# Kernel tuning notes

Measured on AMD Instinct MI355X. Metric: run time of the kernel, lower is better.

Reference implementation:

```python
import jax, jax.numpy as jnp
import numpy as np

IN_DIM, OUT_DIM = 96, 32
D = IN_DIM + OUT_DIM  # 128, feature dim of x
H, KQ = 8, 64         # head_num, KQ_dim
GAMMA = 1e-4


def setup_inputs() -> dict:
    key = jax.random.key(0)
    kx, kk, kq, kv = jax.random.split(key, 4)
    B, N = 32, 2048
    std_kq = (GAMMA / D) ** 0.5
    return {
        "x": jax.random.normal(kx, (B, N, D), dtype=jnp.float32),
        # nn.Linear weight shape [out_features, in_features]; stacked per head
        "Wk": jax.random.normal(kk, (H, KQ, D), dtype=jnp.float32) * std_kq,
        "Wq": jax.random.normal(kq, (H, KQ, D), dtype=jnp.float32) * std_kq,
        "Wv": jax.random.normal(kv, (H, D, D), dtype=jnp.float32) * GAMMA,
    }


def reference(x, Wk, Wq, Wv):
    # Per-head projections (nn.Linear: y = x @ W^T), stacked over heads h
    K = jnp.einsum("bnd,hkd->bhnk", x, Wk)  # [B,H,N,KQ]
    Q = jnp.einsum("bnd,hkd->bhnk", x, Wq)  # [B,H,N,KQ]
    V = jnp.einsum("bnd,hed->bhne", x, Wv)  # [B,H,N,D]
    # No softmax -> (Q K^T) V == Q (K^T V); use the O(n d^2) associative form
    KtV = jnp.einsum("bhnk,bhne->bhke", K, V)  # [B,H,KQ,D]
    # sum over heads folded into the contraction
    out = jnp.einsum("bhnk,bhke->bne", Q, KtV)  # [B,N,D]
    return out
```

## Files before the change

### kernel.cpp

```cpp
#include <hip/hip_runtime.h>

#define BB 32
#define NN 2048
#define DD 128
#define HH 8
#define KK 64

typedef __attribute__((ext_vector_type(8))) short bf16x8;
typedef __attribute__((ext_vector_type(4))) float f32x4;
#define MFMA_BF16 __builtin_amdgcn_mfma_f32_16x16x32_bf16


__device__ __forceinline__ float bf2f(unsigned short h){ return __uint_as_float(((unsigned)h) << 16); }
__device__ __forceinline__ unsigned short f2bf(float f){
  unsigned u = __float_as_uint(f);
  u += 0x7fffu + ((u >> 16) & 1u);
  return (unsigned short)(u >> 16);
}

__device__ __forceinline__ bf16x8 ldfrag_sw(const unsigned short* base, int row16, int kc, int lane){
  int d = row16 + (lane & 15);
  int q = lane >> 4;
  int ch = ((kc << 2) + q) ^ (d & 7);
  return *(const bf16x8*)(base + d*128 + ch*8);
}
__device__ __forceinline__ bf16x8 ldfrag_pad(const unsigned short* base, int row16, int kc, int lane){
  int r = row16 + (lane & 15);
  int q = lane >> 4;
  return *(const bf16x8*)(base + r*136 + kc*32 + q*8);
}

__global__ __launch_bounds__(256) void kgkp(const float* __restrict__ x,
                                            const float* __restrict__ Wq,
                                            const float* __restrict__ Wk,
                                            float* __restrict__ Gp,
                                            unsigned short* __restrict__ Pbf){
  __shared__ __align__(16) unsigned short sm[32768];
  const int t = threadIdx.x;
  const int bid = blockIdx.x;
  if (bid < 512){
    unsigned short* xh = sm;
    unsigned short* xl = sm + 16384;
    const int b = bid & 31, chunk = bid >> 5;
    const float* xb = x + ((size_t)b*NN + (size_t)chunk*128)*DD;
    for (int it = 0; it < 4; ++it){
      int gidx = it*256 + t;
      int n4g = (gidx & 7) | (((gidx >> 6) & 3) << 3);
      int dcq = ((gidx >> 3) & 7) | (((gidx >> 8) & 3) << 3);
      float4 v[4];
      #pragma unroll
      for (int j = 0; j < 4; ++j)
        v[j] = *(const float4*)(xb + (size_t)(n4g*4 + j)*DD + dcq*4);
      #pragma unroll
      for (int i = 0; i < 4; ++i){
        int d = dcq*4 + i;
        float f0 = (&v[0].x)[i], f1 = (&v[1].x)[i], f2 = (&v[2].x)[i], f3 = (&v[3].x)[i];
        unsigned short h0 = f2bf(f0), h1 = f2bf(f1), h2 = f2bf(f2), h3 = f2bf(f3);
        unsigned short l0 = f2bf(f0 - bf2f(h0)), l1 = f2bf(f1 - bf2f(h1));
        unsigned short l2 = f2bf(f2 - bf2f(h2)), l3 = f2bf(f3 - bf2f(h3));
        int off = d*128 + ((((n4g >> 1) ^ (d & 7)) << 3) + (n4g & 1)*4);
        *(ushort4*)(xh + off) = make_ushort4(h0, h1, h2, h3);
        *(ushort4*)(xl + off) = make_ushort4(l0, l1, l2, l3);
      }
    }
    __syncthreads();
    const int w = t >> 6, lane = t & 63, quad = lane >> 4;
    const int wr = (w >> 1)*64, wc = (w & 1)*64;
    f32x4 acc[4][4] = {};
    for (int kc = 0; kc < 4; ++kc){
      bf16x8 ah[4], al[4], bh[4], bl[4];
      #pragma unroll
      for (int r = 0; r < 4; ++r){
        ah[r] = ldfrag_sw(xh, wr + r*16, kc, lane);
        al[r] = ldfrag_sw(xl, wr + r*16, kc, lane);
      }
      #pragma unroll
      for (int c = 0; c < 4; ++c){
        bh[c] = ldfrag_sw(xh, wc + c*16, kc, lane);
        bl[c] = ldfrag_sw(xl, wc + c*16, kc, lane);
      }
      #pragma unroll
      for (int r = 0; r < 4; ++r)
        #pragma unroll
        for (int c = 0; c < 4; ++c){
          acc[r][c] = MFMA_BF16(ah[r], bh[c], acc[r][c], 0, 0, 0);
          acc[r][c] = MFMA_BF16(ah[r], bl[c], acc[r][c], 0, 0, 0);
          acc[r][c] = MFMA_BF16(al[r], bh[c], acc[r][c], 0, 0, 0);
        }
    }
    float* gp = Gp + ((size_t)(chunk*32 + b) << 14);
    #pragma unroll
    for (int r = 0; r < 4; ++r)
      #pragma unroll
      for (int c = 0; c < 4; ++c)
        #pragma unroll
        for (int reg = 0; reg < 4; ++reg)
          gp[(size_t)(wr + r*16 + quad*4 + reg)*DD + wc + c*16 + (lane & 15)] = acc[r][c][reg];
  } else {
    float* Aq = (float*)sm;
    float* Bk = Aq + 64*36;
    const int kpid = bid - 512;
    const int h = kpid >> 2, rt = kpid & 3;
    const int i0 = rt * 32;
    const int tr = t >> 5, tc = t & 31;
    const float* wq = Wq + h*KK*DD;
    const float* wk = Wk + h*KK*DD;
    for (int i = t; i < 512; i += 256){
      int k = i >> 3, c4 = (i & 7) << 2;
      *(float4*)(&Aq[k*36 + c4]) = *(const float4*)(wq + k*DD + i0 + c4);
    }
    for (int i = t; i < 2048; i += 256){
      int k = i >> 5, c4 = (i & 31) << 2;
      *(float4*)(&Bk[k*132 + c4]) = *(const float4*)(wk + k*DD + c4);
    }
    __syncthreads();
    float acc[4][4] = {};
    for (int k = 0; k < 64; k += 2){
      float a0[4], b0[4], a1[4], b1[4];
      *(float4*)a0 = *(float4*)(&Aq[k*36 + tr*4]);
      *(float4*)b0 = *(float4*)(&Bk[k*132 + tc*4]);
      *(float4*)a1 = *(float4*)(&Aq[(k+1)*36 + tr*4]);
      *(float4*)b1 = *(float4*)(&Bk[(k+1)*132 + tc*4]);
      #pragma unroll
      for (int i = 0; i < 4; ++i)
        #pragma unroll
        for (int j = 0; j < 4; ++j){
          acc[i][j] += a0[i]*b0[j];
          acc[i][j] += a1[i]*b1[j];
        }
    }
    unsigned short* Ph = Pbf + h*DD*DD;
    #pragma unroll
    for (int i = 0; i < 4; ++i)
      *(ushort4*)(&Ph[(i0 + tr*4 + i)*DD + tc*4]) =
          make_ushort4(f2bf(acc[i][0]), f2bf(acc[i][1]), f2bf(acc[i][2]), f2bf(acc[i][3]));
  }
}

__global__ __launch_bounds__(256) void kgr(const float* __restrict__ Gp,
                                           unsigned short* __restrict__ Gbf){
  size_t idx = (size_t)blockIdx.x*1024 + threadIdx.x*4;
  int b = (int)(idx >> 14); int i = (int)(idx & 16383);
  float4 s = make_float4(0.f, 0.f, 0.f, 0.f);
  #pragma unroll
  for (int p = 0; p < 16; ++p){
    float4 v = *(const float4*)(Gp + ((size_t)(p*32 + b) << 14) + i);
    s.x += v.x; s.y += v.y; s.z += v.z; s.w += v.w;
  }
  *(ushort4*)(Gbf + idx) = make_ushort4(f2bf(s.x), f2bf(s.y), f2bf(s.z), f2bf(s.w));
}

__global__ __launch_bounds__(256) void km(const unsigned short* __restrict__ Gbf,
                                          const float* __restrict__ Wv,
                                          const unsigned short* __restrict__ Pbf,
                                          float* __restrict__ Mpt){
  __shared__ __align__(16) unsigned short As[128*136];
  __shared__ __align__(16) unsigned short Bs[64*136];
  const int bid = blockIdx.x;
  const int b = bid & 31, h = (bid >> 5) & 7, eh = bid >> 8;
  const int e0 = eh * 64;
  const int t = threadIdx.x;
  const int w = t >> 6, lane = t & 63, quad = lane >> 4;
  const unsigned short* Gb = Gbf + ((size_t)b << 14);
  const float* Wvh = Wv + ((size_t)h*DD + e0)*DD;
  for (int i = t; i < 2048; i += 256){
    int r = i >> 4, ch = (i & 15) * 8;
    *(uint4*)(As + r*136 + ch) = *(const uint4*)(Gb + r*128 + ch);
  }
  for (int i = t; i < 2048; i += 256){
    int e = i >> 5, dc = (i & 31) * 4;
    float4 v = *(const float4*)(Wvh + (size_t)e*DD + dc);
    *(ushort4*)(Bs + e*136 + dc) = make_ushort4(f2bf(v.x), f2bf(v.y), f2bf(v.z), f2bf(v.w));
  }
  __syncthreads();
  const int wr = (w >> 1)*64, wc = (w & 1)*32;
  f32x4 acc1[4][2] = {};
  for (int kc = 0; kc < 4; ++kc){
    bf16x8 a[4], bb[2];
    #pragma unroll
    for (int r = 0; r < 4; ++r) a[r] = ldfrag_pad(As, wr + r*16, kc, lane);
    #pragma unroll
    for (int c = 0; c < 2; ++c) bb[c] = ldfrag_pad(Bs, wc + c*16, kc, lane);
    #pragma unroll
    for (int r = 0; r < 4; ++r)
      #pragma unroll
      for (int c = 0; c < 2; ++c)
        acc1[r][c] = MFMA_BF16(a[r], bb[c], acc1[r][c], 0, 0, 0);
  }
  __syncthreads();
  #pragma unroll
  for (int r = 0; r < 4; ++r)
    #pragma unroll
    for (int c = 0; c < 2; ++c){
      int e = wc + c*16 + (lane & 15);
      int c0 = wr + r*16 + quad*4;
      *(ushort4*)(Bs + e*136 + c0) = make_ushort4(f2bf(acc1[r][c][0]), f2bf(acc1[r][c][1]),
                                                  f2bf(acc1[r][c][2]), f2bf(acc1[r][c][3]));
    }
  const unsigned short* Ph = Pbf + h*DD*DD;
  for (int i = t; i < 2048; i += 256){
    int r = i >> 4, ch = (i & 15) * 8;
    *(uint4*)(As + r*136 + ch) = *(const uint4*)(Ph + r*128 + ch);
  }
  __syncthreads();
  f32x4 acc2[4][2] = {};
  for (int kc = 0; kc < 4; ++kc){
    bf16x8 a[4], bb[2];
    #pragma unroll
    for (int r = 0; r < 4; ++r) a[r] = ldfrag_pad(As, wr + r*16, kc, lane);
    #pragma unroll
    for (int c = 0; c < 2; ++c) bb[c] = ldfrag_pad(Bs, wc + c*16, kc, lane);
    #pragma unroll
    for (int r = 0; r < 4; ++r)
      #pragma unroll
      for (int c = 0; c < 2; ++c)
        acc2[r][c] = MFMA_BF16(a[r], bb[c], acc2[r][c], 0, 0, 0);
  }
  __syncthreads();
  float* Af = (float*)As;
  #pragma unroll
  for (int r = 0; r < 4; ++r)
    #pragma unroll
    for (int c = 0; c < 2; ++c){
      int e = wc + c*16 + (lane & 15);
      int d0 = wr + r*16 + quad*4;
      *(float4*)(Af + e*132 + d0) = make_float4(acc2[r][c][0], acc2[r][c][1], acc2[r][c][2], acc2[r][c][3]);
    }
  __syncthreads();
  float* Mb = Mpt + ((size_t)(b*8 + h) << 14);
  for (int i = t; i < 2048; i += 256){
    int e = i >> 5, dc = (i & 31) * 4;
    *(float4*)(Mb + (size_t)(e0 + e)*DD + dc) = *(const float4*)(Af + e*132 + dc);
  }
}

__global__ __launch_bounds__(256) void kmr(const float* __restrict__ Mpt,
                                           unsigned short* __restrict__ Mtbf){
  size_t idx = (size_t)blockIdx.x*1024 + threadIdx.x*4;
  int b = (int)(idx >> 14); int i = (int)(idx & 16383);
  float4 s = make_float4(0.f, 0.f, 0.f, 0.f);
  #pragma unroll
  for (int h = 0; h < 8; ++h){
    float4 v = *(const float4*)(Mpt + ((size_t)(b*8 + h) << 14) + i);
    s.x += v.x; s.y += v.y; s.z += v.z; s.w += v.w;
  }
  *(ushort4*)(Mtbf + idx) = make_ushort4(f2bf(s.x), f2bf(s.y), f2bf(s.z), f2bf(s.w));
}

__global__ __launch_bounds__(256) void ko(const float* __restrict__ x,
                                          const unsigned short* __restrict__ Mtbf,
                                          float* __restrict__ out){
  __shared__ __align__(16) unsigned short xs[16384];
  __shared__ __align__(16) unsigned short Ms[16384];
  const int bid = blockIdx.x;
  const int b = bid & 31, nt = bid >> 5;
  const int t = threadIdx.x;
  const int w = t >> 6, lane = t & 63, quad = lane >> 4;
  const float* xb = x + ((size_t)b*NN + (size_t)nt*128)*DD;
  const unsigned short* Mtb = Mtbf + ((size_t)b << 14);
  for (int i = t; i < 4096; i += 256){
    int n = i >> 5, dcq = i & 31;
    float4 v = *(const float4*)(xb + (size_t)n*DD + dcq*4);
    int off = n*128 + ((((dcq >> 1) ^ (n & 7)) << 3) + (dcq & 1)*4);
    *(ushort4*)(xs + off) = make_ushort4(f2bf(v.x), f2bf(v.y), f2bf(v.z), f2bf(v.w));
  }
  for (int i = t; i < 2048; i += 256){
    int e = i >> 4, ng = i & 15;
    *(uint4*)(Ms + e*128 + ((ng ^ (e & 7)) << 3)) = *(const uint4*)(Mtb + e*128 + ng*8);
  }
  __syncthreads();
  const int wr = (w >> 1)*64, wc = (w & 1)*64;
  f32x4 acc[4][4] = {};
  for (int kc = 0; kc < 4; ++kc){
    bf16x8 a[4], bb[4];
    #pragma unroll
    for (int r = 0; r < 4; ++r) a[r] = ldfrag_sw(xs, wr + r*16, kc, lane);
    #pragma unroll
    for (int c = 0; c < 4; ++c) bb[c] = ldfrag_sw(Ms, wc + c*16, kc, lane);
    #pragma unroll
    for (int r = 0; r < 4; ++r)
      #pragma unroll
      for (int c = 0; c < 4; ++c)
        acc[r][c] = MFMA_BF16(a[r], bb[c], acc[r][c], 0, 0, 0);
  }
  float* ob = out + ((size_t)b*NN + (size_t)nt*128)*DD;
  #pragma unroll
  for (int r = 0; r < 4; ++r)
    #pragma unroll
    for (int c = 0; c < 4; ++c)
      #pragma unroll
      for (int reg = 0; reg < 4; ++reg)
        ob[(size_t)(wr + r*16 + quad*4 + reg)*DD + wc + c*16 + (lane & 15)] = acc[r][c][reg];
}

extern "C" void kernel_launch(void* const* d_in, const int* in_sizes, int n_in,
                              void* d_out, int out_size, void* d_ws, size_t ws_size,
                              hipStream_t stream){
  const float* x  = (const float*)d_in[0];
  const float* Wk = (const float*)d_in[1];
  const float* Wq = (const float*)d_in[2];
  const float* Wv = (const float*)d_in[3];
  float* out = (float*)d_out;
  float* ws = (float*)d_ws;
  float* Gp  = ws;
  float* Mpt = ws + 8388608;
  unsigned short* Gbf  = (unsigned short*)(ws + 12582912);
  unsigned short* Pbf  = Gbf + 524288;
  unsigned short* Mtbf = Pbf + 131072;

  kgkp<<<544, 256, 0, stream>>>(x, Wq, Wk, Gp, Pbf);
  kgr <<<512, 256, 0, stream>>>(Gp, Gbf);
  km  <<<512, 256, 0, stream>>>(Gbf, Wv, Pbf, Mpt);
  kmr <<<512, 256, 0, stream>>>(Mpt, Mtbf);
  ko  <<<512, 256, 0, stream>>>(x, Mtbf, out);
}
```

Measured before the change: 128.1 us.

## Fuse partial-sum reductions into consumers and store partials in bf16

Removes the two standalone reduction kernels. The Gram and head partial sums are now summed inside the consuming kernels (km2 and ko2) as they load their tiles. The partial buffers are stored as bf16 instead of fp32, which halves that traffic, and output writes go through LDS so they can be coalesced as float4. In exchange, each km2 and ko2 block redundantly re-reads all partials for its batch, and rounding the partials to bf16 adds precision loss before summation.

```diff
diff --git a/kernel.cpp b/kernel.cpp
--- a/kernel.cpp
+++ b/kernel.cpp
@@ -33,7 +33,7 @@
 __global__ __launch_bounds__(256) void kgkp(const float* __restrict__ x,
                                             const float* __restrict__ Wq,
                                             const float* __restrict__ Wk,
-                                            float* __restrict__ Gp,
+                                            unsigned short* __restrict__ Gp_bf,
                                             unsigned short* __restrict__ Pbf){
   __shared__ __align__(16) unsigned short sm[32768];
   const int t = threadIdx.x;
@@ -88,14 +88,25 @@
           acc[r][c] = MFMA_BF16(al[r], bh[c], acc[r][c], 0, 0, 0);
         }
     }
-    float* gp = Gp + ((size_t)(chunk*32 + b) << 14);
+    __syncthreads();
+    float* Sf = (float*)sm;
     #pragma unroll
     for (int r = 0; r < 4; ++r)
       #pragma unroll
       for (int c = 0; c < 4; ++c)
         #pragma unroll
         for (int reg = 0; reg < 4; ++reg)
-          gp[(size_t)(wr + r*16 + quad*4 + reg)*DD + wc + c*16 + (lane & 15)] = acc[r][c][reg];
+          Sf[(wr + r*16 + quad*4 + reg)*128 + wc + c*16 + (lane & 15)] = acc[r][c][reg];
+    __syncthreads();
+    unsigned short* gp = Gp_bf + ((size_t)(chunk*32 + b) << 14);
+    for (int i = t; i < 2048; i += 256){
+      int r = i >> 4, c8 = (i & 15) * 8;
+      const float* s = Sf + r*128 + c8;
+      ushort4 lo = make_ushort4(f2bf(s[0]), f2bf(s[1]), f2bf(s[2]), f2bf(s[3]));
+      ushort4 hi = make_ushort4(f2bf(s[4]), f2bf(s[5]), f2bf(s[6]), f2bf(s[7]));
+      *(ushort4*)(gp + r*128 + c8)     = lo;
+      *(ushort4*)(gp + r*128 + c8 + 4) = hi;
+    }
   } else {
     float* Aq = (float*)sm;
     float* Bk = Aq + 64*36;
@@ -137,23 +148,10 @@
   }
 }
 
-__global__ __launch_bounds__(256) void kgr(const float* __restrict__ Gp,
-                                           unsigned short* __restrict__ Gbf){
-  size_t idx = (size_t)blockIdx.x*1024 + threadIdx.x*4;
-  int b = (int)(idx >> 14); int i = (int)(idx & 16383);
-  float4 s = make_float4(0.f, 0.f, 0.f, 0.f);
-  #pragma unroll
-  for (int p = 0; p < 16; ++p){
-    float4 v = *(const float4*)(Gp + ((size_t)(p*32 + b) << 14) + i);
-    s.x += v.x; s.y += v.y; s.z += v.z; s.w += v.w;
-  }
-  *(ushort4*)(Gbf + idx) = make_ushort4(f2bf(s.x), f2bf(s.y), f2bf(s.z), f2bf(s.w));
-}
-
-__global__ __launch_bounds__(256) void km(const unsigned short* __restrict__ Gbf,
-                                          const float* __restrict__ Wv,
-                                          const unsigned short* __restrict__ Pbf,
-                                          float* __restrict__ Mpt){
+__global__ __launch_bounds__(256) void km2(const unsigned short* __restrict__ Gp_bf,
+                                           const float* __restrict__ Wv,
+                                           const unsigned short* __restrict__ Pbf,
+                                           unsigned short* __restrict__ Mpt_bf){
   __shared__ __align__(16) unsigned short As[128*136];
   __shared__ __align__(16) unsigned short Bs[64*136];
   const int bid = blockIdx.x;
@@ -161,12 +159,22 @@
   const int e0 = eh * 64;
   const int t = threadIdx.x;
   const int w = t >> 6, lane = t & 63, quad = lane >> 4;
-  const unsigned short* Gb = Gbf + ((size_t)b << 14);
+  for (int i = t; i < 2048; i += 256){
+    int r = i >> 4, c8 = (i & 15) * 8;
+    float s[8] = {};
+    #pragma unroll
+    for (int p = 0; p < 16; ++p){
+      uint4 u = *(const uint4*)(Gp_bf + (((size_t)(p*32 + b)) << 14) + r*128 + c8);
+      const unsigned short* pu = (const unsigned short*)&u;
+      #pragma unroll
+      for (int j = 0; j < 8; ++j) s[j] += bf2f(pu[j]);
+    }
+    ushort4 lo = make_ushort4(f2bf(s[0]), f2bf(s[1]), f2bf(s[2]), f2bf(s[3]));
+    ushort4 hi = make_ushort4(f2bf(s[4]), f2bf(s[5]), f2bf(s[6]), f2bf(s[7]));
+    *(ushort4*)(As + r*136 + c8)     = lo;
+    *(ushort4*)(As + r*136 + c8 + 4) = hi;
+  }
   const float* Wvh = Wv + ((size_t)h*DD + e0)*DD;
-  for (int i = t; i < 2048; i += 256){
-    int r = i >> 4, ch = (i & 15) * 8;
-    *(uint4*)(As + r*136 + ch) = *(const uint4*)(Gb + r*128 + ch);
-  }
   for (int i = t; i < 2048; i += 256){
     int e = i >> 5, dc = (i & 31) * 4;
     float4 v = *(const float4*)(Wvh + (size_t)e*DD + dc);
@@ -227,37 +235,28 @@
       *(float4*)(Af + e*132 + d0) = make_float4(acc2[r][c][0], acc2[r][c][1], acc2[r][c][2], acc2[r][c][3]);
     }
   __syncthreads();
-  float* Mb = Mpt + ((size_t)(b*8 + h) << 14);
-  for (int i = t; i < 2048; i += 256){
-    int e = i >> 5, dc = (i & 31) * 4;
-    *(float4*)(Mb + (size_t)(e0 + e)*DD + dc) = *(const float4*)(Af + e*132 + dc);
-  }
-}
-
-__global__ __launch_bounds__(256) void kmr(const float* __restrict__ Mpt,
-                                           unsigned short* __restrict__ Mtbf){
-  size_t idx = (size_t)blockIdx.x*1024 + threadIdx.x*4;
-  int b = (int)(idx >> 14); int i = (int)(idx & 16383);
-  float4 s = make_float4(0.f, 0.f, 0.f, 0.f);
-  #pragma unroll
-  for (int h = 0; h < 8; ++h){
-    float4 v = *(const float4*)(Mpt + ((size_t)(b*8 + h) << 14) + i);
-    s.x += v.x; s.y += v.y; s.z += v.z; s.w += v.w;
-  }
-  *(ushort4*)(Mtbf + idx) = make_ushort4(f2bf(s.x), f2bf(s.y), f2bf(s.z), f2bf(s.w));
-}
-
-__global__ __launch_bounds__(256) void ko(const float* __restrict__ x,
-                                          const unsigned short* __restrict__ Mtbf,
-                                          float* __restrict__ out){
-  __shared__ __align__(16) unsigned short xs[16384];
-  __shared__ __align__(16) unsigned short Ms[16384];
+  unsigned short* Mb = Mpt_bf + (((size_t)(b*8 + h)) << 14);
+  for (int i = t; i < 1024; i += 256){
+    int e = i >> 4, c8 = (i & 15) * 8;
+    const float* s = Af + e*132 + c8;
+    ushort4 lo = make_ushort4(f2bf(s[0]), f2bf(s[1]), f2bf(s[2]), f2bf(s[3]));
+    ushort4 hi = make_ushort4(f2bf(s[4]), f2bf(s[5]), f2bf(s[6]), f2bf(s[7]));
+    *(ushort4*)(Mb + (e0 + e)*128 + c8)     = lo;
+    *(ushort4*)(Mb + (e0 + e)*128 + c8 + 4) = hi;
+  }
+}
+
+__global__ __launch_bounds__(256) void ko2(const float* __restrict__ x,
+                                           const unsigned short* __restrict__ Mpt_bf,
+                                           float* __restrict__ out){
+  __shared__ __align__(16) unsigned short sm[32768];
+  unsigned short* xs = sm;
+  unsigned short* Ms = sm + 16384;
   const int bid = blockIdx.x;
   const int b = bid & 31, nt = bid >> 5;
   const int t = threadIdx.x;
   const int w = t >> 6, lane = t & 63, quad = lane >> 4;
   const float* xb = x + ((size_t)b*NN + (size_t)nt*128)*DD;
-  const unsigned short* Mtb = Mtbf + ((size_t)b << 14);
   for (int i = t; i < 4096; i += 256){
     int n = i >> 5, dcq = i & 31;
     float4 v = *(const float4*)(xb + (size_t)n*DD + dcq*4);
@@ -265,8 +264,18 @@
     *(ushort4*)(xs + off) = make_ushort4(f2bf(v.x), f2bf(v.y), f2bf(v.z), f2bf(v.w));
   }
   for (int i = t; i < 2048; i += 256){
-    int e = i >> 4, ng = i & 15;
-    *(uint4*)(Ms + e*128 + ((ng ^ (e & 7)) << 3)) = *(const uint4*)(Mtb + e*128 + ng*8);
+    int e = i >> 4, c8 = (i & 15) * 8;
+    float s[8] = {};
+    #pragma unroll
+    for (int h = 0; h < 8; ++h){
+      uint4 u = *(const uint4*)(Mpt_bf + (((size_t)(b*8 + h)) << 14) + e*128 + c8);
+      const unsigned short* pu = (const unsigned short*)&u;
+      #pragma unroll
+      for (int j = 0; j < 8; ++j) s[j] += bf2f(pu[j]);
+    }
+    int off = e*128 + (((c8 >> 3) ^ (e & 7)) << 3);
+    *(ushort4*)(Ms + off)     = make_ushort4(f2bf(s[0]), f2bf(s[1]), f2bf(s[2]), f2bf(s[3]));
+    *(ushort4*)(Ms + off + 4) = make_ushort4(f2bf(s[4]), f2bf(s[5]), f2bf(s[6]), f2bf(s[7]));
   }
   __syncthreads();
   const int wr = (w >> 1)*64, wc = (w & 1)*64;
@@ -283,14 +292,21 @@
       for (int c = 0; c < 4; ++c)
         acc[r][c] = MFMA_BF16(a[r], bb[c], acc[r][c], 0, 0, 0);
   }
-  float* ob = out + ((size_t)b*NN + (size_t)nt*128)*DD;
+  __syncthreads();
+  float* Sf = (float*)sm;
   #pragma unroll
   for (int r = 0; r < 4; ++r)
     #pragma unroll
     for (int c = 0; c < 4; ++c)
       #pragma unroll
       for (int reg = 0; reg < 4; ++reg)
-        ob[(size_t)(wr + r*16 + quad*4 + reg)*DD + wc + c*16 + (lane & 15)] = acc[r][c][reg];
+        Sf[(wr + r*16 + quad*4 + reg)*128 + wc + c*16 + (lane & 15)] = acc[r][c][reg];
+  __syncthreads();
+  float* ob = out + ((size_t)b*NN + (size_t)nt*128)*DD;
+  for (int i = t; i < 4096; i += 256){
+    int n = i >> 5, c4 = (i & 31) * 4;
+    *(float4*)(ob + (size_t)n*DD + c4) = *(const float4*)(Sf + n*128 + c4);
+  }
 }
 
 extern "C" void kernel_launch(void* const* d_in, const int* in_sizes, int n_in,
@@ -302,15 +318,11 @@
   const float* Wv = (const float*)d_in[3];
   float* out = (float*)d_out;
   float* ws = (float*)d_ws;
-  float* Gp  = ws;
-  float* Mpt = ws + 8388608;
-  unsigned short* Gbf  = (unsigned short*)(ws + 12582912);
-  unsigned short* Pbf  = Gbf + 524288;
-  unsigned short* Mtbf = Pbf + 131072;
-
-  kgkp<<<544, 256, 0, stream>>>(x, Wq, Wk, Gp, Pbf);
-  kgr <<<512, 256, 0, stream>>>(Gp, Gbf);
-  km  <<<512, 256, 0, stream>>>(Gbf, Wv, Pbf, Mpt);
-  kmr <<<512, 256, 0, stream>>>(Mpt, Mtbf);
-  ko  <<<512, 256, 0, stream>>>(x, Mtbf, out);
-}
+  unsigned short* Gp_bf  = (unsigned short*)ws;
+  unsigned short* Mpt_bf = (unsigned short*)(ws + 4194304);
+  unsigned short* Pbf    = (unsigned short*)(ws + 6291456);
+
+  kgkp<<<544, 256, 0, stream>>>(x, Wq, Wk, Gp_bf, Pbf);
+  km2 <<<512, 256, 0, stream>>>(Gp_bf, Wv, Pbf, Mpt_bf);
+  ko2 <<<512, 256, 0, stream>>>(x, Mpt_bf, out);
+}
```

Result: no change. 129.4 us (+1.0%).
